# Optimization experiments

Hardware: AMD Instinct MI355X
Metric: run time of the kernel (lower is better)

## Reference

```python
import jax, jax.numpy as jnp
import numpy as np

VOCAB, H1, H2 = 50257, 1024, 512


def gru_cell(x, h, w_ih, w_hh, b_ih, b_hh):
    # PyTorch GRU cell math. x: [B, Din], h: [B, H]
    gx = x @ w_ih.T + b_ih          # [B, 3H]
    gh = h @ w_hh.T + b_hh          # [B, 3H]
    xr, xz, xn = jnp.split(gx, 3, axis=-1)
    hr, hz, hn = jnp.split(gh, 3, axis=-1)
    r = jax.nn.sigmoid(xr + hr)
    z = jax.nn.sigmoid(xz + hz)
    n = jnp.tanh(xn + r * hn)
    return (1.0 - z) * n + z * h


def setup_inputs() -> dict:
    key = jax.random.key(0)
    ks = jax.random.split(key, 12)
    s1 = 1.0 / np.sqrt(H1)
    s2 = 1.0 / np.sqrt(H2)
    return {
        "input_ids": jax.random.randint(ks[0], (1,), 0, VOCAB),
        "hidden_1": jax.random.normal(ks[1], (1, 1, H1), dtype=jnp.float32),
        "hidden_2": jax.random.normal(ks[2], (1, 1, H2), dtype=jnp.float32),
        "emb": jax.random.normal(ks[3], (VOCAB, H1), dtype=jnp.float32),
        "w_ih1": jax.random.uniform(ks[4], (3 * H1, H1), jnp.float32, -s1, s1),
        "w_hh1": jax.random.uniform(ks[5], (3 * H1, H1), jnp.float32, -s1, s1),
        "b_ih1": jax.random.uniform(ks[6], (3 * H1,), jnp.float32, -s1, s1),
        "b_hh1": jax.random.uniform(ks[7], (3 * H1,), jnp.float32, -s1, s1),
        "w_ih2": jax.random.uniform(ks[8], (3 * H2, H1), jnp.float32, -s2, s2),
        "w_hh2": jax.random.uniform(ks[9], (3 * H2, H2), jnp.float32, -s2, s2),
        "b_ih2": jax.random.uniform(ks[10], (3 * H2,), jnp.float32, -s2, s2),
        "b_hh2": jax.random.uniform(ks[11], (3 * H2,), jnp.float32, -s2, s2),
    }


def reference(input_ids, hidden_1, hidden_2, emb, w_ih1, w_hh1, b_ih1, b_hh1,
              w_ih2, w_hh2, b_ih2, b_hh2):
    # Embedding lookup -> [1, H1] (seq=1, batch=1 collapsed to one row)
    x = emb[input_ids].reshape(1, H1)
    h1 = gru_cell(x, hidden_1.reshape(1, H1), w_ih1, w_hh1, b_ih1, b_hh1)
    h2 = gru_cell(h1, hidden_2.reshape(1, H2), w_ih2, w_hh2, b_ih2, b_hh2)
    output = h2.reshape(1, 1, H2)
    return output, h1.reshape(1, 1, H1), h2.reshape(1, 1, H2)
```

## Files before the change

kernel.cpp:

```cpp
#include <hip/hip_runtime.h>
#include <math.h>

#define H1 1024
#define H2 512
#define NB_H1 1024
#define NB_GH2 384
#define NB_K1 (NB_H1 + NB_GH2)

__device__ __forceinline__ float sigmoidf_(float x) { return 1.0f / (1.0f + __expf(-x)); }
__device__ __forceinline__ float dot4(float4 a, float4 b) {
    return a.x * b.x + a.y * b.y + a.z * b.z + a.w * b.w;
}
__device__ __forceinline__ float wave_sum(float v) {
#pragma unroll
    for (int o = 32; o; o >>= 1) v += __shfl_xor(v, o, 64);
    return v;
}

__global__ __launch_bounds__(256) void gru_k1(
    const int* __restrict__ ids,
    const float* __restrict__ h1_in,
    const float* __restrict__ h2_in,
    const float* __restrict__ emb,
    const float* __restrict__ w_ih1,
    const float* __restrict__ w_hh1,
    const float* __restrict__ b_ih1,
    const float* __restrict__ b_hh1,
    const float* __restrict__ w_hh2,
    const float* __restrict__ b_hh2,
    float* __restrict__ d_out,
    float* __restrict__ gh2_ws)
{
    const int t = threadIdx.x;
    const int wave = t >> 6, lane = t & 63;
    const int b = blockIdx.x;

    if (b < NB_H1) {
        __shared__ float red[6][4];
        const int j = b;
        const float bxr = b_ih1[j], bxz = b_ih1[j + H1], bxn = b_ih1[j + 2 * H1];
        const float bhr = b_hh1[j], bhz = b_hh1[j + H1], bhn = b_hh1[j + 2 * H1];
        const float hprev = h1_in[j];

        const float* xrow = emb + (size_t)ids[0] * H1;
        const float4 x4 = ((const float4*)xrow)[t];
        const float4 h4 = ((const float4*)h1_in)[t];

        float acc[6];
#pragma unroll
        for (int g = 0; g < 3; ++g) {
            const float4 a = ((const float4*)(w_ih1 + (size_t)(g * H1 + j) * H1))[t];
            const float4 c = ((const float4*)(w_hh1 + (size_t)(g * H1 + j) * H1))[t];
            acc[g]     = dot4(x4, a);
            acc[3 + g] = dot4(h4, c);
        }
#pragma unroll
        for (int g = 0; g < 6; ++g) {
            const float v = wave_sum(acc[g]);
            if (lane == 0) red[g][wave] = v;
        }
        __syncthreads();
        if (t == 0) {
            float s[6];
#pragma unroll
            for (int g = 0; g < 6; ++g)
                s[g] = red[g][0] + red[g][1] + red[g][2] + red[g][3];
            const float r = sigmoidf_(s[0] + bxr + s[3] + bhr);
            const float z = sigmoidf_(s[1] + bxz + s[4] + bhz);
            const float n = tanhf(s[2] + bxn + r * (s[5] + bhn));
            d_out[H2 + j] = (1.0f - z) * n + z * hprev;
        }
    } else {
        const int row = (b - NB_H1) * 4 + wave;
        const float bias = b_hh2[row];
        float acc = 0.0f;
#pragma unroll
        for (int k = 0; k < 2; ++k) {
            const int idx = lane + 64 * k;
            const float4 h4 = ((const float4*)h2_in)[idx];
            const float4 wv = ((const float4*)(w_hh2 + (size_t)row * H2))[idx];
            acc += dot4(h4, wv);
        }
        acc = wave_sum(acc);
        if (lane == 0) gh2_ws[row] = acc + bias;
    }
}

__global__ __launch_bounds__(256) void gru_k2(
    const float* __restrict__ h2_in,
    const float* __restrict__ w_ih2,
    const float* __restrict__ b_ih2,
    const float* __restrict__ gh2_ws,
    float* __restrict__ d_out)
{
    __shared__ float red[3][4];
    const int t = threadIdx.x;
    const int wave = t >> 6, lane = t & 63;
    const int j = blockIdx.x;

    const float bxr = b_ih2[j], bxz = b_ih2[j + H2], bxn = b_ih2[j + 2 * H2];
    const float hr = gh2_ws[j], hz = gh2_ws[j + H2], hn = gh2_ws[j + 2 * H2];
    const float hprev = h2_in[j];

    const float* h1v = d_out + H2;
    const float4 hh = ((const float4*)h1v)[t];

    float acc[3];
#pragma unroll
    for (int g = 0; g < 3; ++g) {
        const float4 a = ((const float4*)(w_ih2 + (size_t)(g * H2 + j) * H1))[t];
        acc[g] = dot4(hh, a);
    }
#pragma unroll
    for (int g = 0; g < 3; ++g) {
        const float v = wave_sum(acc[g]);
        if (lane == 0) red[g][wave] = v;
    }
    __syncthreads();
    if (t == 0) {
        const float gx0 = red[0][0] + red[0][1] + red[0][2] + red[0][3];
        const float gx1 = red[1][0] + red[1][1] + red[1][2] + red[1][3];
        const float gx2 = red[2][0] + red[2][1] + red[2][2] + red[2][3];
        const float r = sigmoidf_(gx0 + bxr + hr);
        const float z = sigmoidf_(gx1 + bxz + hz);
        const float n = tanhf(gx2 + bxn + r * hn);
        const float h = (1.0f - z) * n + z * hprev;
        d_out[j] = h;
        d_out[3 * H2 + j] = h;
    }
}

extern "C" void kernel_launch(void* const* d_in, const int* in_sizes, int n_in,
                              void* d_out, int out_size, void* d_ws, size_t ws_size,
                              hipStream_t stream) {
    const int*   ids   = (const int*)d_in[0];
    const float* h1_in = (const float*)d_in[1];
    const float* h2_in = (const float*)d_in[2];
    const float* emb   = (const float*)d_in[3];
    const float* w_ih1 = (const float*)d_in[4];
    const float* w_hh1 = (const float*)d_in[5];
    const float* b_ih1 = (const float*)d_in[6];
    const float* b_hh1 = (const float*)d_in[7];
    const float* w_ih2 = (const float*)d_in[8];
    const float* w_hh2 = (const float*)d_in[9];
    const float* b_ih2 = (const float*)d_in[10];
    const float* b_hh2 = (const float*)d_in[11];
    float* out = (float*)d_out;
    float* gh2 = (float*)d_ws;

    gru_k1<<<NB_K1, 256, 0, stream>>>(ids, h1_in, h2_in, emb,
                                      w_ih1, w_hh1, b_ih1, b_hh1,
                                      w_hh2, b_hh2, out, gh2);
    gru_k2<<<H2, 256, 0, stream>>>(h2_in, w_ih2, b_ih2, gh2, out);
}
```

Before: 13.74 us.

## Fuse both GRU layers into one kernel with a grid-wide atomic barrier

Measured after the change: 34.05 us. 148% more time.

```diff
diff --git a/kernel.cpp b/kernel.cpp
--- a/kernel.cpp
+++ b/kernel.cpp
@@ -3,9 +3,10 @@
 
 #define H1 1024
 #define H2 512
-#define NB_H1 1024
-#define NB_GH2 384
-#define NB_K1 (NB_H1 + NB_GH2)
+#define NBLK 640
+#define NSLOT 64
+#define SLOT_STRIDE 16
+
 
 __device__ __forceinline__ float sigmoidf_(float x) { return 1.0f / (1.0f + __expf(-x)); }
 __device__ __forceinline__ float dot4(float4 a, float4 b) {
@@ -17,7 +18,7 @@
     return v;
 }
 
-__global__ __launch_bounds__(256) void gru_k1(
+__global__ __launch_bounds__(256, 4) void gru_one(
     const int* __restrict__ ids,
     const float* __restrict__ h1_in,
     const float* __restrict__ h2_in,
@@ -26,52 +27,53 @@
     const float* __restrict__ w_hh1,
     const float* __restrict__ b_ih1,
     const float* __restrict__ b_hh1,
+    const float* __restrict__ w_ih2,
     const float* __restrict__ w_hh2,
+    const float* __restrict__ b_ih2,
     const float* __restrict__ b_hh2,
     float* __restrict__ d_out,
-    float* __restrict__ gh2_ws)
+    unsigned int* __restrict__ ws_u)
 {
     const int t = threadIdx.x;
-    const int wave = t >> 6, lane = t & 63;
+    const int wid = t >> 6, lane = t & 63;
     const int b = blockIdx.x;
+    const int g = b * 4 + wid;
 
-    if (b < NB_H1) {
-        __shared__ float red[6][4];
-        const int j = b;
+    unsigned int* slots = ws_u;
+    unsigned int* dflag = ws_u + 1024;
+    float* gh2 = (float*)(ws_u + 1152);
+
+    if (g < H1) {
+        const int j = g;
         const float bxr = b_ih1[j], bxz = b_ih1[j + H1], bxn = b_ih1[j + 2 * H1];
         const float bhr = b_hh1[j], bhz = b_hh1[j + H1], bhn = b_hh1[j + 2 * H1];
         const float hprev = h1_in[j];
-
         const float* xrow = emb + (size_t)ids[0] * H1;
-        const float4 x4 = ((const float4*)xrow)[t];
-        const float4 h4 = ((const float4*)h1_in)[t];
-
-        float acc[6];
+        float acc[6] = {0, 0, 0, 0, 0, 0};
 #pragma unroll
-        for (int g = 0; g < 3; ++g) {
-            const float4 a = ((const float4*)(w_ih1 + (size_t)(g * H1 + j) * H1))[t];
-            const float4 c = ((const float4*)(w_hh1 + (size_t)(g * H1 + j) * H1))[t];
-            acc[g]     = dot4(x4, a);
-            acc[3 + g] = dot4(h4, c);
+        for (int k = 0; k < 4; ++k) {
+            const int idx = lane + 64 * k;
+            const float4 x4 = ((const float4*)xrow)[idx];
+            const float4 h4 = ((const float4*)h1_in)[idx];
+#pragma unroll
+            for (int gg = 0; gg < 3; ++gg) {
+                const float4 a = ((const float4*)(w_ih1 + (size_t)(gg * H1 + j) * H1))[idx];
+                const float4 c = ((const float4*)(w_hh1 + (size_t)(gg * H1 + j) * H1))[idx];
+                acc[gg]     += dot4(x4, a);
+                acc[3 + gg] += dot4(h4, c);
+            }
         }
 #pragma unroll
-        for (int g = 0; g < 6; ++g) {
-            const float v = wave_sum(acc[g]);
-            if (lane == 0) red[g][wave] = v;
-        }
-        __syncthreads();
-        if (t == 0) {
-            float s[6];
-#pragma unroll
-            for (int g = 0; g < 6; ++g)
-                s[g] = red[g][0] + red[g][1] + red[g][2] + red[g][3];
-            const float r = sigmoidf_(s[0] + bxr + s[3] + bhr);
-            const float z = sigmoidf_(s[1] + bxz + s[4] + bhz);
-            const float n = tanhf(s[2] + bxn + r * (s[5] + bhn));
-            d_out[H2 + j] = (1.0f - z) * n + z * hprev;
+        for (int gg = 0; gg < 6; ++gg) acc[gg] = wave_sum(acc[gg]);
+        if (lane == 0) {
+            const float r = sigmoidf_(acc[0] + bxr + acc[3] + bhr);
+            const float z = sigmoidf_(acc[1] + bxz + acc[4] + bhz);
+            const float n = tanhf(acc[2] + bxn + r * (acc[5] + bhn));
+            const float h = (1.0f - z) * n + z * hprev;
+            __hip_atomic_store(&d_out[H2 + j], h, __ATOMIC_RELAXED, __HIP_MEMORY_SCOPE_AGENT);
         }
     } else {
-        const int row = (b - NB_H1) * 4 + wave;
+        const int row = g - H1;
         const float bias = b_hh2[row];
         float acc = 0.0f;
 #pragma unroll
@@ -82,49 +84,72 @@
             acc += dot4(h4, wv);
         }
         acc = wave_sum(acc);
-        if (lane == 0) gh2_ws[row] = acc + bias;
+        if (lane == 0)
+            __hip_atomic_store(&gh2[row], acc + bias, __ATOMIC_RELAXED, __HIP_MEMORY_SCOPE_AGENT);
     }
-}
 
-__global__ __launch_bounds__(256) void gru_k2(
-    const float* __restrict__ h2_in,
-    const float* __restrict__ w_ih2,
-    const float* __restrict__ b_ih2,
-    const float* __restrict__ gh2_ws,
-    float* __restrict__ d_out)
-{
+    asm volatile("s_waitcnt vmcnt(0)" ::: "memory");
+    __syncthreads();
+    if (t == 0)
+        __hip_atomic_fetch_add(&slots[(b & (NSLOT - 1)) * SLOT_STRIDE], 1u,
+                               __ATOMIC_RELAXED, __HIP_MEMORY_SCOPE_AGENT);
+    if (b >= H2) return;
+
+    if (b < 8 && t == 0) {
+        for (;;) {
+            unsigned s = 0;
+#pragma unroll 1
+            for (int i = 0; i < NSLOT; ++i)
+                s += __hip_atomic_load(&slots[i * SLOT_STRIDE],
+                                       __ATOMIC_RELAXED, __HIP_MEMORY_SCOPE_AGENT);
+            if (s == (unsigned)NBLK) break;
+            __builtin_amdgcn_s_sleep(8);
+        }
+        __hip_atomic_store(dflag, 1u, __ATOMIC_RELAXED, __HIP_MEMORY_SCOPE_AGENT);
+    }
+    if (t == 0) {
+        while (__hip_atomic_load(dflag, __ATOMIC_RELAXED, __HIP_MEMORY_SCOPE_AGENT) == 0u)
+            __builtin_amdgcn_s_sleep(4);
+    }
+    __syncthreads();
+
     __shared__ float red[3][4];
-    const int t = threadIdx.x;
-    const int wave = t >> 6, lane = t & 63;
-    const int j = blockIdx.x;
+    __shared__ float shg[3];
+    const int j = b;
+    const float bxr2 = b_ih2[j], bxz2 = b_ih2[j + H2], bxn2 = b_ih2[j + 2 * H2];
+    const float hprev2 = h2_in[j];
+    if (t < 3)
+        shg[t] = __hip_atomic_load(&gh2[j + H2 * t], __ATOMIC_RELAXED, __HIP_MEMORY_SCOPE_AGENT);
 
-    const float bxr = b_ih2[j], bxz = b_ih2[j + H2], bxn = b_ih2[j + 2 * H2];
-    const float hr = gh2_ws[j], hz = gh2_ws[j + H2], hn = gh2_ws[j + 2 * H2];
-    const float hprev = h2_in[j];
+    unsigned long long* h1u = (unsigned long long*)(d_out + H2);
+    const unsigned long long u0 =
+        __hip_atomic_load(&h1u[2 * t + 0], __ATOMIC_RELAXED, __HIP_MEMORY_SCOPE_AGENT);
+    const unsigned long long u1 =
+        __hip_atomic_load(&h1u[2 * t + 1], __ATOMIC_RELAXED, __HIP_MEMORY_SCOPE_AGENT);
+    union { unsigned long long u; float f[2]; } c0, c1;
+    c0.u = u0; c1.u = u1;
+    const float4 hh = make_float4(c0.f[0], c0.f[1], c1.f[0], c1.f[1]);
 
-    const float* h1v = d_out + H2;
-    const float4 hh = ((const float4*)h1v)[t];
-
-    float acc[3];
+    float a3[3];
 #pragma unroll
-    for (int g = 0; g < 3; ++g) {
-        const float4 a = ((const float4*)(w_ih2 + (size_t)(g * H2 + j) * H1))[t];
-        acc[g] = dot4(hh, a);
+    for (int gg = 0; gg < 3; ++gg) {
+        const float4 a = ((const float4*)(w_ih2 + (size_t)(gg * H2 + j) * H1))[t];
+        a3[gg] = dot4(hh, a);
     }
 #pragma unroll
-    for (int g = 0; g < 3; ++g) {
-        const float v = wave_sum(acc[g]);
-        if (lane == 0) red[g][wave] = v;
+    for (int gg = 0; gg < 3; ++gg) {
+        const float v = wave_sum(a3[gg]);
+        if (lane == 0) red[gg][wid] = v;
     }
     __syncthreads();
     if (t == 0) {
         const float gx0 = red[0][0] + red[0][1] + red[0][2] + red[0][3];
         const float gx1 = red[1][0] + red[1][1] + red[1][2] + red[1][3];
         const float gx2 = red[2][0] + red[2][1] + red[2][2] + red[2][3];
-        const float r = sigmoidf_(gx0 + bxr + hr);
-        const float z = sigmoidf_(gx1 + bxz + hz);
-        const float n = tanhf(gx2 + bxn + r * hn);
-        const float h = (1.0f - z) * n + z * hprev;
+        const float r = sigmoidf_(gx0 + bxr2 + shg[0]);
+        const float z = sigmoidf_(gx1 + bxz2 + shg[1]);
+        const float n = tanhf(gx2 + bxn2 + r * shg[2]);
+        const float h = (1.0f - z) * n + z * hprev2;
         d_out[j] = h;
         d_out[3 * H2 + j] = h;
     }
@@ -145,11 +170,10 @@
     const float* w_hh2 = (const float*)d_in[9];
     const float* b_ih2 = (const float*)d_in[10];
     const float* b_hh2 = (const float*)d_in[11];
-    float* out = (float*)d_out;
-    float* gh2 = (float*)d_ws;
 
-    gru_k1<<<NB_K1, 256, 0, stream>>>(ids, h1_in, h2_in, emb,
+    hipMemsetAsync(d_ws, 0, 4608, stream);
+    gru_one<<<NBLK, 256, 0, stream>>>(ids, h1_in, h2_in, emb,
                                       w_ih1, w_hh1, b_ih1, b_hh1,
-                                      w_hh2, b_hh2, out, gh2);
-    gru_k2<<<H2, 256, 0, stream>>>(h2_in, w_ih2, b_ih2, gh2, out);
+                                      w_ih2, w_hh2, b_ih2, b_hh2,
+                                      (float*)d_out, (unsigned int*)d_ws);
 }
```

## Map one hidden unit per wave in layer 1 and fold hidden-gate GEMV into layer 2

Applied to the files above, without the earlier changes.

Measured after the change: 13.38 us, median of 2. -2.6%, faster.

```diff
diff --git a/kernel.cpp b/kernel.cpp
--- a/kernel.cpp
+++ b/kernel.cpp
@@ -3,12 +3,12 @@
 
 #define H1 1024
 #define H2 512
-#define NB_H1 1024
-#define NB_GH2 384
-#define NB_K1 (NB_H1 + NB_GH2)
+
+typedef float vfloat4 __attribute__((ext_vector_type(4)));
+typedef float vfloat2 __attribute__((ext_vector_type(2)));
 
 __device__ __forceinline__ float sigmoidf_(float x) { return 1.0f / (1.0f + __expf(-x)); }
-__device__ __forceinline__ float dot4(float4 a, float4 b) {
+__device__ __forceinline__ float dot4(float4 a, vfloat4 b) {
     return a.x * b.x + a.y * b.y + a.z * b.z + a.w * b.w;
 }
 __device__ __forceinline__ float wave_sum(float v) {
@@ -16,114 +16,98 @@
     for (int o = 32; o; o >>= 1) v += __shfl_xor(v, o, 64);
     return v;
 }
+__device__ __forceinline__ vfloat4 ntload4(const float* p) {
+    return __builtin_nontemporal_load((const vfloat4*)p);
+}
+__device__ __forceinline__ vfloat2 ntload2(const float* p) {
+    return __builtin_nontemporal_load((const vfloat2*)p);
+}
 
 __global__ __launch_bounds__(256) void gru_k1(
     const int* __restrict__ ids,
     const float* __restrict__ h1_in,
-    const float* __restrict__ h2_in,
     const float* __restrict__ emb,
     const float* __restrict__ w_ih1,
     const float* __restrict__ w_hh1,
     const float* __restrict__ b_ih1,
     const float* __restrict__ b_hh1,
-    const float* __restrict__ w_hh2,
-    const float* __restrict__ b_hh2,
-    float* __restrict__ d_out,
-    float* __restrict__ gh2_ws)
+    float* __restrict__ d_out)
 {
-    const int t = threadIdx.x;
-    const int wave = t >> 6, lane = t & 63;
-    const int b = blockIdx.x;
+    const int lane = threadIdx.x & 63;
+    const int j = blockIdx.x * 4 + (threadIdx.x >> 6);
 
-    if (b < NB_H1) {
-        __shared__ float red[6][4];
-        const int j = b;
-        const float bxr = b_ih1[j], bxz = b_ih1[j + H1], bxn = b_ih1[j + 2 * H1];
-        const float bhr = b_hh1[j], bhz = b_hh1[j + H1], bhn = b_hh1[j + 2 * H1];
-        const float hprev = h1_in[j];
+    const float bxr = b_ih1[j], bxz = b_ih1[j + H1], bxn = b_ih1[j + 2 * H1];
+    const float bhr = b_hh1[j], bhz = b_hh1[j + H1], bhn = b_hh1[j + 2 * H1];
+    const float hprev = h1_in[j];
+    const float* xrow = emb + (size_t)ids[0] * H1;
 
-        const float* xrow = emb + (size_t)ids[0] * H1;
-        const float4 x4 = ((const float4*)xrow)[t];
-        const float4 h4 = ((const float4*)h1_in)[t];
-
-        float acc[6];
+    float acc[6] = {0, 0, 0, 0, 0, 0};
+#pragma unroll
+    for (int k = 0; k < 4; ++k) {
+        const int idx = lane + 64 * k;
+        const float4 x4 = ((const float4*)xrow)[idx];
+        const float4 h4 = ((const float4*)h1_in)[idx];
 #pragma unroll
         for (int g = 0; g < 3; ++g) {
-            const float4 a = ((const float4*)(w_ih1 + (size_t)(g * H1 + j) * H1))[t];
-            const float4 c = ((const float4*)(w_hh1 + (size_t)(g * H1 + j) * H1))[t];
-            acc[g]     = dot4(x4, a);
-            acc[3 + g] = dot4(h4, c);
+            const vfloat4 a = ntload4(w_ih1 + (size_t)(g * H1 + j) * H1 + 4 * idx);
+            const vfloat4 c = ntload4(w_hh1 + (size_t)(g * H1 + j) * H1 + 4 * idx);
+            acc[g]     += dot4(x4, a);
+            acc[3 + g] += dot4(h4, c);
         }
+    }
 #pragma unroll
-        for (int g = 0; g < 6; ++g) {
-            const float v = wave_sum(acc[g]);
-            if (lane == 0) red[g][wave] = v;
-        }
-        __syncthreads();
-        if (t == 0) {
-            float s[6];
-#pragma unroll
-            for (int g = 0; g < 6; ++g)
-                s[g] = red[g][0] + red[g][1] + red[g][2] + red[g][3];
-            const float r = sigmoidf_(s[0] + bxr + s[3] + bhr);
-            const float z = sigmoidf_(s[1] + bxz + s[4] + bhz);
-            const float n = tanhf(s[2] + bxn + r * (s[5] + bhn));
-            d_out[H2 + j] = (1.0f - z) * n + z * hprev;
-        }
-    } else {
-        const int row = (b - NB_H1) * 4 + wave;
-        const float bias = b_hh2[row];
-        float acc = 0.0f;
-#pragma unroll
-        for (int k = 0; k < 2; ++k) {
-            const int idx = lane + 64 * k;
-            const float4 h4 = ((const float4*)h2_in)[idx];
-            const float4 wv = ((const float4*)(w_hh2 + (size_t)row * H2))[idx];
-            acc += dot4(h4, wv);
-        }
-        acc = wave_sum(acc);
-        if (lane == 0) gh2_ws[row] = acc + bias;
+    for (int g = 0; g < 6; ++g) acc[g] = wave_sum(acc[g]);
+    if (lane == 0) {
+        const float r = sigmoidf_(acc[0] + bxr + acc[3] + bhr);
+        const float z = sigmoidf_(acc[1] + bxz + acc[4] + bhz);
+        const float n = tanhf(acc[2] + bxn + r * (acc[5] + bhn));
+        d_out[H2 + j] = (1.0f - z) * n + z * hprev;
     }
 }
 
 __global__ __launch_bounds__(256) void gru_k2(
     const float* __restrict__ h2_in,
     const float* __restrict__ w_ih2,
+    const float* __restrict__ w_hh2,
     const float* __restrict__ b_ih2,
-    const float* __restrict__ gh2_ws,
+    const float* __restrict__ b_hh2,
     float* __restrict__ d_out)
 {
-    __shared__ float red[3][4];
+    __shared__ float red[6][4];
     const int t = threadIdx.x;
-    const int wave = t >> 6, lane = t & 63;
+    const int wid = t >> 6, lane = t & 63;
     const int j = blockIdx.x;
 
     const float bxr = b_ih2[j], bxz = b_ih2[j + H2], bxn = b_ih2[j + 2 * H2];
-    const float hr = gh2_ws[j], hz = gh2_ws[j + H2], hn = gh2_ws[j + 2 * H2];
+    const float bhr = b_hh2[j], bhz = b_hh2[j + H2], bhn = b_hh2[j + 2 * H2];
     const float hprev = h2_in[j];
 
     const float* h1v = d_out + H2;
     const float4 hh = ((const float4*)h1v)[t];
+    const float2 h2v = ((const float2*)h2_in)[t];
 
-    float acc[3];
+    float acc[6];
 #pragma unroll
     for (int g = 0; g < 3; ++g) {
-        const float4 a = ((const float4*)(w_ih2 + (size_t)(g * H2 + j) * H1))[t];
-        acc[g] = dot4(hh, a);
+        const vfloat4 a = ntload4(w_ih2 + (size_t)(g * H2 + j) * H1 + 4 * t);
+        const vfloat2 c = ntload2(w_hh2 + (size_t)(g * H2 + j) * H2 + 2 * t);
+        acc[g]     = dot4(hh, a);
+        acc[3 + g] = h2v.x * c.x + h2v.y * c.y;
     }
 #pragma unroll
-    for (int g = 0; g < 3; ++g) {
+    for (int g = 0; g < 6; ++g) {
         const float v = wave_sum(acc[g]);
-        if (lane == 0) red[g][wave] = v;
+        if (lane == 0) red[g][wid] = v;
     }
     __syncthreads();
     if (t == 0) {
-        const float gx0 = red[0][0] + red[0][1] + red[0][2] + red[0][3];
-        const float gx1 = red[1][0] + red[1][1] + red[1][2] + red[1][3];
-        const float gx2 = red[2][0] + red[2][1] + red[2][2] + red[2][3];
-        const float r = sigmoidf_(gx0 + bxr + hr);
-        const float z = sigmoidf_(gx1 + bxz + hz);
-        const float n = tanhf(gx2 + bxn + r * hn);
+        float s[6];
+#pragma unroll
+        for (int g = 0; g < 6; ++g)
+            s[g] = red[g][0] + red[g][1] + red[g][2] + red[g][3];
+        const float r = sigmoidf_(s[0] + bxr + s[3] + bhr);
+        const float z = sigmoidf_(s[1] + bxz + s[4] + bhz);
+        const float n = tanhf(s[2] + bxn + r * (s[5] + bhn));
         const float h = (1.0f - z) * n + z * hprev;
         d_out[j] = h;
         d_out[3 * H2 + j] = h;
@@ -146,10 +130,7 @@
     const float* b_ih2 = (const float*)d_in[10];
     const float* b_hh2 = (const float*)d_in[11];
     float* out = (float*)d_out;
-    float* gh2 = (float*)d_ws;
 
-    gru_k1<<<NB_K1, 256, 0, stream>>>(ids, h1_in, h2_in, emb,
-                                      w_ih1, w_hh1, b_ih1, b_hh1,
-                                      w_hh2, b_hh2, out, gh2);
-    gru_k2<<<H2, 256, 0, stream>>>(h2_in, w_ih2, b_ih2, gh2, out);
+    gru_k1<<<H1 / 4, 256, 0, stream>>>(ids, h1_in, emb, w_ih1, w_hh1, b_ih1, b_hh1, out);
+    gru_k2<<<H2, 256, 0, stream>>>(h2_in, w_ih2, w_hh2, b_ih2, b_hh2, out);
 }
```
